# Performance work log

Measured on AMD Instinct MI355X. Metric: run time of the kernel, lower is better.

Reference implementation:

```python
import jax, jax.numpy as jnp
import numpy as np

N_QUBITS = 4
N_LAYERS = 3
DIM = 2 ** N_QUBITS  # 16 amplitudes; qubit 0 is the most-significant bit
BATCH = 262144

# bit of qubit q in basis index: (idx >> (N_QUBITS-1-q)) & 1
_bits = (np.arange(DIM)[:, None] >> np.arange(N_QUBITS - 1, -1, -1)[None, :]) & 1  # [16,4]

# circular CZ entangler diagonal: CZ(0,1),CZ(1,2),CZ(2,3),CZ(0,3)
_sign = np.ones(DIM)
for p, q in [(0, 1), (1, 2), (2, 3), (0, 3)]:
    _sign *= 1.0 - 2.0 * (_bits[:, p] * _bits[:, q])
CZ_DIAG = jnp.asarray(_sign, jnp.complex64)           # [16]
ZMAT = jnp.asarray(1 - 2 * _bits, jnp.float32)        # [16,4], <Z_q> signs


def _rx(t):
    c = jnp.cos(t / 2).astype(jnp.complex64)
    js = (-1j) * jnp.sin(t / 2).astype(jnp.complex64)
    return jnp.stack([jnp.stack([c, js], -1), jnp.stack([js, c], -1)], -2)


def _ry(t):
    c = jnp.cos(t / 2).astype(jnp.complex64)
    s = jnp.sin(t / 2).astype(jnp.complex64)
    return jnp.stack([jnp.stack([c, -s], -1), jnp.stack([s, c], -1)], -2)


def _rz(t):
    ph = jnp.exp(-0.5j * t.astype(jnp.complex64))
    z = jnp.zeros_like(ph)
    return jnp.stack([jnp.stack([ph, z], -1), jnp.stack([z, jnp.conj(ph)], -1)], -2)


def _apply(psi, M, q):
    # psi: [B, 16] complex64, M: [2,2] (shared) or [B,2,2] (per-sample)
    L, R = 2 ** q, 2 ** (N_QUBITS - 1 - q)
    B = psi.shape[0]
    psi = psi.reshape(B, L, 2, R)
    eq = 'ij,bljr->blir' if M.ndim == 2 else 'bij,bljr->blir'
    return jnp.einsum(eq, M, psi).reshape(B, DIM)


def setup_inputs() -> dict:
    key = jax.random.key(0)
    k1, k2 = jax.random.split(key)
    x = jax.random.normal(k1, (BATCH, N_QUBITS), dtype=jnp.float32)
    theta = jax.random.uniform(k2, (1, 3 * (N_LAYERS + 1) * N_QUBITS),
                               minval=0.0, maxval=np.pi, dtype=jnp.float32)
    lmbd = jnp.ones((N_QUBITS * N_LAYERS,), dtype=jnp.float32)
    return {"x": x, "theta": theta, "lmbd": lmbd}


def reference(x, theta, lmbd):
    B = x.shape[0]
    params = theta.reshape(N_LAYERS + 1, N_QUBITS, 3)
    # tiled inputs scaled by trainable lambdas: a[b,l,i] = lmbd[l*4+i] * x[b,i]
    a = lmbd.reshape(N_LAYERS, N_QUBITS)[None] * x[:, None, :]  # [B,3,4]
    # activation = 'linear' -> identity
    psi = jnp.zeros((B, DIM), jnp.complex64).at[:, 0].set(1.0)
    for l in range(N_LAYERS):
        # variational single-qubit rotations (shared across batch)
        for i in range(N_QUBITS):
            psi = _apply(psi, _rx(params[l, i, 0]), i)
            psi = _apply(psi, _ry(params[l, i, 1]), i)
            psi = _apply(psi, _rz(params[l, i, 2]), i)
        # circular CZ entangler (diagonal)
        psi = psi * CZ_DIAG
        # data re-uploading (per-sample angles)
        for i in range(N_QUBITS):
            psi = _apply(psi, _rx(a[:, l, i]), i)
        for i in range(N_QUBITS):
            psi = _apply(psi, _ry(a[:, l, i]), i)
        zang = (a[:, l, 0], a[:, l, 0], a[:, l, 1], a[:, l, 1])
        for i in range(N_QUBITS):
            psi = _apply(psi, _rz(zang[i]), i)
        # trailing variational rotations with last-layer params (applied every layer)
        for i in range(N_QUBITS):
            psi = _apply(psi, _rx(params[N_LAYERS, i, 0]), i)
            psi = _apply(psi, _ry(params[N_LAYERS, i, 1]), i)
            psi = _apply(psi, _rz(params[N_LAYERS, i, 2]), i)
    probs = psi.real ** 2 + psi.imag ** 2  # [B,16]
    return probs @ ZMAT                    # [B,4] <Z_q> expectations
```

## Files before the change

### kernel.cpp

```cpp
#include <hip/hip_runtime.h>

#define BATCH 262144
#define BLOCK 256

typedef float v2 __attribute__((ext_vector_type(2)));

struct c2f { float re, im; };

__device__ __forceinline__ c2f cmul(c2f a, c2f b){
    return { a.re*b.re - a.im*b.im, a.re*b.im + a.im*b.re };
}
__device__ __forceinline__ c2f cmulc(c2f a, c2f b){
    return { a.re*b.re + a.im*b.im, a.im*b.re - a.re*b.im };
}
__device__ __forceinline__ void su2mul(c2f a1, c2f b1, c2f a2, c2f b2, c2f& ao, c2f& bo){
    c2f t1 = cmul(a1, a2), t2 = cmulc(b1, b2);
    ao = { t1.re - t2.re, t1.im - t2.im };
    c2f t3 = cmul(a1, b2), t4 = cmulc(b1, a2);
    bo = { t3.re + t4.re, t3.im + t4.im };
}
__device__ __forceinline__ int czneg(int s){
    int b0 = (s >> 3) & 1, b1 = (s >> 2) & 1, b2 = (s >> 1) & 1, b3 = s & 1;
    return (b0 & b1) ^ (b1 & b2) ^ (b2 & b3) ^ (b0 & b3);
}

__device__ __forceinline__ v2 pkfma(v2 a, v2 b, v2 c){
    return __builtin_elementwise_fma(a, b, c);
}

__global__ __launch_bounds__(BLOCK) void vqc_kernel(
    const float* __restrict__ x,
    const float* __restrict__ theta,
    const float* __restrict__ lmbd,
    float* __restrict__ out)
{
    const int tid = threadIdx.x;
    const int b = blockIdx.x * BLOCK + tid;
    const float4 xr = ((const float4*)x)[b];

    __shared__ float2 sU[4][4][2];
    __shared__ float2 sA[3][4][2];
    __shared__ float2 sPsi0[16];
    __shared__ float  sL[12];

    if (tid < 16) {
        int l = tid >> 2, q = tid & 3;
        float t0 = 0.5f * theta[(l * 4 + q) * 3 + 0];
        float t1 = 0.5f * theta[(l * 4 + q) * 3 + 1];
        float t2 = 0.5f * theta[(l * 4 + q) * 3 + 2];
        float c0, s0, c1, s1, c2v, s2v;
        __sincosf(t0, &s0, &c0);
        __sincosf(t1, &s1, &c1);
        __sincosf(t2, &s2v, &c2v);
        c2f aP = { c1 * c0, s1 * s0 };
        c2f bP = { -s1 * c0, -c1 * s0 };
        c2f ph = { c2v, -s2v };
        c2f aU = cmul(ph, aP);
        c2f bU = cmul(ph, bP);
        sU[l][q][0] = make_float2(aU.re, aU.im);
        sU[l][q][1] = make_float2(bU.re, bU.im);
    }
    if (tid < 12) sL[tid] = lmbd[tid];
    __syncthreads();

    if (tid < 12) {
        int k = tid >> 2, q = tid & 3;
        c2f aW = { sU[3][q][0].x, sU[3][q][0].y };
        c2f bW = { sU[3][q][1].x, sU[3][q][1].y };
        c2f aA = aW, bA = bW;
        if (k < 2) {
            c2f aN = { sU[k + 1][q][0].x, sU[k + 1][q][0].y };
            c2f bN = { sU[k + 1][q][1].x, sU[k + 1][q][1].y };
            su2mul(aN, bN, aW, bW, aA, bA);
        }
        sA[k][q][0] = make_float2(aA.re, aA.im);
        sA[k][q][1] = make_float2(bA.re, bA.im);
    }
    if (tid >= 16 && tid < 32) {
        int s = tid - 16;
        c2f v = { 1.f, 0.f };
        #pragma unroll
        for (int q = 0; q < 4; ++q) {
            int bit = (s >> (3 - q)) & 1;
            c2f a = { sU[0][q][0].x, sU[0][q][0].y };
            c2f b2 = { sU[0][q][1].x, sU[0][q][1].y };
            c2f e = bit ? c2f{ -b2.re, b2.im } : a;
            v = cmul(v, e);
        }
        if (czneg(s)) { v.re = -v.re; v.im = -v.im; }
        sPsi0[s] = make_float2(v.re, v.im);
    }
    __syncthreads();


#define DECLP(n) v2 p##n = { sPsi0[n].x, sPsi0[n].y };
    DECLP(0)  DECLP(1)  DECLP(2)  DECLP(3)
    DECLP(4)  DECLP(5)  DECLP(6)  DECLP(7)
    DECLP(8)  DECLP(9)  DECLP(10) DECLP(11)
    DECLP(12) DECLP(13) DECLP(14) DECLP(15)
#undef DECLP

#define BF(n0,n1) { \
    const v2 q0 = p##n0, q1 = p##n1; \
    const v2 r0 = { -q0.y, q0.x }; \
    const v2 r1 = { -q1.y, q1.x }; \
    v2 t0 = bMi2 * r1; \
    t0 = pkfma(bMr2, q1, t0); \
    t0 = pkfma(aMi2, r0, t0); \
    t0 = pkfma(aMr2, q0, t0); \
    v2 t1 = bMi2 * r0; \
    t1 = pkfma(bMr2, -q0, t1); \
    t1 = pkfma(aMi2, -r1, t1); \
    t1 = pkfma(aMr2, q1, t1); \
    p##n0 = t0; p##n1 = t1; \
}

#define GATE(kk,qq,zq,...) { \
    const float c_ = ch##qq, s_ = sh##qq; \
    const float cz_ = ch##zq, sz_ = sh##zq; \
    const float cc_ = c_*c_, ss_ = s_*s_, cs_ = c_*s_; \
    const float aVr = cc_*cz_ + ss_*sz_, aVi = ss_*cz_ - cc_*sz_; \
    const float bVr = -cs_*(cz_+sz_),  bVi = -cs_*(cz_-sz_); \
    const float2 fa = sA[kk][qq][0], fb = sA[kk][qq][1]; \
    const float aMr = fa.x*aVr - fa.y*aVi - (fb.x*bVr + fb.y*bVi); \
    const float aMi = fa.x*aVi + fa.y*aVr - (fb.y*bVr - fb.x*bVi); \
    const float bMr = fa.x*bVr - fa.y*bVi + (fb.x*aVr + fb.y*aVi); \
    const float bMi = fa.x*bVi + fa.y*bVr + (fb.y*aVr - fb.x*aVi); \
    const v2 aMr2 = { aMr, aMr }, aMi2 = { aMi, aMi }; \
    const v2 bMr2 = { bMr, bMr }, bMi2 = { bMi, bMi }; \
    __VA_ARGS__ \
}

#define CZFLIP \
    p3 = -p3;  p6 = -p6;  p9 = -p9;  p12 = -p12;

#define LAYER(kk, DO_CZ) { \
    const float h0 = 0.5f * sL[kk*4+0] * xr.x; \
    const float h1 = 0.5f * sL[kk*4+1] * xr.y; \
    const float h2 = 0.5f * sL[kk*4+2] * xr.z; \
    const float h3 = 0.5f * sL[kk*4+3] * xr.w; \
    float ch0, sh0, ch1, sh1, ch2, sh2, ch3, sh3; \
    __sincosf(h0, &sh0, &ch0); \
    __sincosf(h1, &sh1, &ch1); \
    __sincosf(h2, &sh2, &ch2); \
    __sincosf(h3, &sh3, &ch3); \
    GATE(kk,0,0, BF(0,8)  BF(1,9)  BF(2,10) BF(3,11) BF(4,12) BF(5,13) BF(6,14)  BF(7,15))  \
    GATE(kk,1,0, BF(0,4)  BF(1,5)  BF(2,6)  BF(3,7)  BF(8,12) BF(9,13) BF(10,14) BF(11,15)) \
    GATE(kk,2,1, BF(0,2)  BF(1,3)  BF(4,6)  BF(5,7)  BF(8,10) BF(9,11) BF(12,14) BF(13,15)) \
    GATE(kk,3,1, BF(0,1)  BF(2,3)  BF(4,5)  BF(6,7)  BF(8,9)  BF(10,11) BF(12,13) BF(14,15))\
    if (DO_CZ) { CZFLIP } \
}

    LAYER(0, 1)
    LAYER(1, 1)
    LAYER(2, 0)

#undef LAYER
#undef GATE
#undef BF
#undef CZFLIP

#define PROB(n) const float m##n = p##n.x*p##n.x + p##n.y*p##n.y;
    PROB(0)  PROB(1)  PROB(2)  PROB(3)
    PROB(4)  PROB(5)  PROB(6)  PROB(7)
    PROB(8)  PROB(9)  PROB(10) PROB(11)
    PROB(12) PROB(13) PROB(14) PROB(15)
#undef PROB

    const float o0 = ((m0+m1)+(m2+m3)+(m4+m5)+(m6+m7))
                   - ((m8+m9)+(m10+m11)+(m12+m13)+(m14+m15));
    const float o1 = ((m0+m1)+(m2+m3)+(m8+m9)+(m10+m11))
                   - ((m4+m5)+(m6+m7)+(m12+m13)+(m14+m15));
    const float o2 = ((m0+m1)+(m4+m5)+(m8+m9)+(m12+m13))
                   - ((m2+m3)+(m6+m7)+(m10+m11)+(m14+m15));
    const float o3 = ((m0+m2)+(m4+m6)+(m8+m10)+(m12+m14))
                   - ((m1+m3)+(m5+m7)+(m9+m11)+(m13+m15));

    ((float4*)out)[b] = make_float4(o0, o1, o2, o3);
}

extern "C" void kernel_launch(void* const* d_in, const int* in_sizes, int n_in,
                              void* d_out, int out_size, void* d_ws, size_t ws_size,
                              hipStream_t stream) {
    const float* x     = (const float*)d_in[0];
    const float* theta = (const float*)d_in[1];
    const float* lmbd  = (const float*)d_in[2];
    float* out = (float*)d_out;
    vqc_kernel<<<dim3(BATCH / BLOCK), dim3(BLOCK), 0, stream>>>(x, theta, lmbd, out);
}
```

Baseline: 71.90 us.

## Process two batch samples per thread and cache gate constants in registers

```diff
diff --git a/kernel.cpp b/kernel.cpp
--- a/kernel.cpp
+++ b/kernel.cpp
@@ -2,6 +2,7 @@
 
 #define BATCH 262144
 #define BLOCK 256
+#define GRID  (BATCH / (BLOCK * 2))
 
 typedef float v2 __attribute__((ext_vector_type(2)));
 
@@ -35,13 +36,15 @@
     float* __restrict__ out)
 {
     const int tid = threadIdx.x;
-    const int b = blockIdx.x * BLOCK + tid;
-    const float4 xr = ((const float4*)x)[b];
+    const int i0 = blockIdx.x * (BLOCK * 2) + tid;
+    const int i1 = i0 + BLOCK;
+    const float4 xrA = ((const float4*)x)[i0];
+    const float4 xrB = ((const float4*)x)[i1];
 
     __shared__ float2 sU[4][4][2];
     __shared__ float2 sA[3][4][2];
     __shared__ float2 sPsi0[16];
-    __shared__ float  sL[12];
+    __shared__ float  sLs[12];
 
     if (tid < 16) {
         int l = tid >> 2, q = tid & 3;
@@ -60,7 +63,7 @@
         sU[l][q][0] = make_float2(aU.re, aU.im);
         sU[l][q][1] = make_float2(bU.re, bU.im);
     }
-    if (tid < 12) sL[tid] = lmbd[tid];
+    if (tid < 12) sLs[tid] = lmbd[tid];
     __syncthreads();
 
     if (tid < 12) {
@@ -92,16 +95,27 @@
     }
     __syncthreads();
 
-
-#define DECLP(n) v2 p##n = { sPsi0[n].x, sPsi0[n].y };
+    float2 rA[3][4][2];
+    #pragma unroll
+    for (int k = 0; k < 3; ++k)
+        #pragma unroll
+        for (int q = 0; q < 4; ++q) {
+            rA[k][q][0] = sA[k][q][0];
+            rA[k][q][1] = sA[k][q][1];
+        }
+    float rL[12];
+    #pragma unroll
+    for (int j = 0; j < 12; ++j) rL[j] = sLs[j];
+
+#define DECLP(n) v2 pA##n = { sPsi0[n].x, sPsi0[n].y }; v2 pB##n = pA##n;
     DECLP(0)  DECLP(1)  DECLP(2)  DECLP(3)
     DECLP(4)  DECLP(5)  DECLP(6)  DECLP(7)
     DECLP(8)  DECLP(9)  DECLP(10) DECLP(11)
     DECLP(12) DECLP(13) DECLP(14) DECLP(15)
 #undef DECLP
 
-#define BF(n0,n1) { \
-    const v2 q0 = p##n0, q1 = p##n1; \
+#define BF(E,n0,n1) { \
+    const v2 q0 = p##E##n0, q1 = p##E##n1; \
     const v2 r0 = { -q0.y, q0.x }; \
     const v2 r1 = { -q1.y, q1.x }; \
     v2 t0 = bMi2 * r1; \
@@ -112,16 +126,16 @@
     t1 = pkfma(bMr2, -q0, t1); \
     t1 = pkfma(aMi2, -r1, t1); \
     t1 = pkfma(aMr2, q1, t1); \
-    p##n0 = t0; p##n1 = t1; \
-}
-
-#define GATE(kk,qq,zq,...) { \
-    const float c_ = ch##qq, s_ = sh##qq; \
-    const float cz_ = ch##zq, sz_ = sh##zq; \
+    p##E##n0 = t0; p##E##n1 = t1; \
+}
+
+#define GATE(E,kk,qq,zq,...) { \
+    const float c_ = ch##E##qq, s_ = sh##E##qq; \
+    const float cz_ = ch##E##zq, sz_ = sh##E##zq; \
     const float cc_ = c_*c_, ss_ = s_*s_, cs_ = c_*s_; \
     const float aVr = cc_*cz_ + ss_*sz_, aVi = ss_*cz_ - cc_*sz_; \
     const float bVr = -cs_*(cz_+sz_),  bVi = -cs_*(cz_-sz_); \
-    const float2 fa = sA[kk][qq][0], fb = sA[kk][qq][1]; \
+    const float2 fa = rA[kk][qq][0], fb = rA[kk][qq][1]; \
     const float aMr = fa.x*aVr - fa.y*aVi - (fb.x*bVr + fb.y*bVi); \
     const float aMi = fa.x*aVi + fa.y*aVr - (fb.y*bVr - fb.x*bVi); \
     const float bMr = fa.x*bVr - fa.y*bVi + (fb.x*aVr + fb.y*aVi); \
@@ -131,24 +145,30 @@
     __VA_ARGS__ \
 }
 
-#define CZFLIP \
-    p3 = -p3;  p6 = -p6;  p9 = -p9;  p12 = -p12;
+#define CZFLIP(E) \
+    p##E##3 = -p##E##3;  p##E##6 = -p##E##6; \
+    p##E##9 = -p##E##9;  p##E##12 = -p##E##12;
 
 #define LAYER(kk, DO_CZ) { \
-    const float h0 = 0.5f * sL[kk*4+0] * xr.x; \
-    const float h1 = 0.5f * sL[kk*4+1] * xr.y; \
-    const float h2 = 0.5f * sL[kk*4+2] * xr.z; \
-    const float h3 = 0.5f * sL[kk*4+3] * xr.w; \
-    float ch0, sh0, ch1, sh1, ch2, sh2, ch3, sh3; \
-    __sincosf(h0, &sh0, &ch0); \
-    __sincosf(h1, &sh1, &ch1); \
-    __sincosf(h2, &sh2, &ch2); \
-    __sincosf(h3, &sh3, &ch3); \
-    GATE(kk,0,0, BF(0,8)  BF(1,9)  BF(2,10) BF(3,11) BF(4,12) BF(5,13) BF(6,14)  BF(7,15))  \
-    GATE(kk,1,0, BF(0,4)  BF(1,5)  BF(2,6)  BF(3,7)  BF(8,12) BF(9,13) BF(10,14) BF(11,15)) \
-    GATE(kk,2,1, BF(0,2)  BF(1,3)  BF(4,6)  BF(5,7)  BF(8,10) BF(9,11) BF(12,14) BF(13,15)) \
-    GATE(kk,3,1, BF(0,1)  BF(2,3)  BF(4,5)  BF(6,7)  BF(8,9)  BF(10,11) BF(12,13) BF(14,15))\
-    if (DO_CZ) { CZFLIP } \
+    float chA0, shA0, chA1, shA1, chA2, shA2, chA3, shA3; \
+    float chB0, shB0, chB1, shB1, chB2, shB2, chB3, shB3; \
+    __sincosf(0.5f * rL[kk*4+0] * xrA.x, &shA0, &chA0); \
+    __sincosf(0.5f * rL[kk*4+1] * xrA.y, &shA1, &chA1); \
+    __sincosf(0.5f * rL[kk*4+2] * xrA.z, &shA2, &chA2); \
+    __sincosf(0.5f * rL[kk*4+3] * xrA.w, &shA3, &chA3); \
+    __sincosf(0.5f * rL[kk*4+0] * xrB.x, &shB0, &chB0); \
+    __sincosf(0.5f * rL[kk*4+1] * xrB.y, &shB1, &chB1); \
+    __sincosf(0.5f * rL[kk*4+2] * xrB.z, &shB2, &chB2); \
+    __sincosf(0.5f * rL[kk*4+3] * xrB.w, &shB3, &chB3); \
+    GATE(A,kk,0,0, BF(A,0,8)  BF(A,1,9)  BF(A,2,10) BF(A,3,11) BF(A,4,12) BF(A,5,13) BF(A,6,14)  BF(A,7,15))  \
+    GATE(B,kk,0,0, BF(B,0,8)  BF(B,1,9)  BF(B,2,10) BF(B,3,11) BF(B,4,12) BF(B,5,13) BF(B,6,14)  BF(B,7,15))  \
+    GATE(A,kk,1,0, BF(A,0,4)  BF(A,1,5)  BF(A,2,6)  BF(A,3,7)  BF(A,8,12) BF(A,9,13) BF(A,10,14) BF(A,11,15)) \
+    GATE(B,kk,1,0, BF(B,0,4)  BF(B,1,5)  BF(B,2,6)  BF(B,3,7)  BF(B,8,12) BF(B,9,13) BF(B,10,14) BF(B,11,15)) \
+    GATE(A,kk,2,1, BF(A,0,2)  BF(A,1,3)  BF(A,4,6)  BF(A,5,7)  BF(A,8,10) BF(A,9,11) BF(A,12,14) BF(A,13,15)) \
+    GATE(B,kk,2,1, BF(B,0,2)  BF(B,1,3)  BF(B,4,6)  BF(B,5,7)  BF(B,8,10) BF(B,9,11) BF(B,12,14) BF(B,13,15)) \
+    GATE(A,kk,3,1, BF(A,0,1)  BF(A,2,3)  BF(A,4,5)  BF(A,6,7)  BF(A,8,9)  BF(A,10,11) BF(A,12,13) BF(A,14,15))\
+    GATE(B,kk,3,1, BF(B,0,1)  BF(B,2,3)  BF(B,4,5)  BF(B,6,7)  BF(B,8,9)  BF(B,10,11) BF(B,12,13) BF(B,14,15))\
+    if (DO_CZ) { CZFLIP(A) CZFLIP(B) } \
 }
 
     LAYER(0, 1)
@@ -160,23 +180,27 @@
 #undef BF
 #undef CZFLIP
 
-#define PROB(n) const float m##n = p##n.x*p##n.x + p##n.y*p##n.y;
-    PROB(0)  PROB(1)  PROB(2)  PROB(3)
-    PROB(4)  PROB(5)  PROB(6)  PROB(7)
-    PROB(8)  PROB(9)  PROB(10) PROB(11)
-    PROB(12) PROB(13) PROB(14) PROB(15)
-#undef PROB
-
-    const float o0 = ((m0+m1)+(m2+m3)+(m4+m5)+(m6+m7))
-                   - ((m8+m9)+(m10+m11)+(m12+m13)+(m14+m15));
-    const float o1 = ((m0+m1)+(m2+m3)+(m8+m9)+(m10+m11))
-                   - ((m4+m5)+(m6+m7)+(m12+m13)+(m14+m15));
-    const float o2 = ((m0+m1)+(m4+m5)+(m8+m9)+(m12+m13))
-                   - ((m2+m3)+(m6+m7)+(m10+m11)+(m14+m15));
-    const float o3 = ((m0+m2)+(m4+m6)+(m8+m10)+(m12+m14))
-                   - ((m1+m3)+(m5+m7)+(m9+m11)+(m13+m15));
-
-    ((float4*)out)[b] = make_float4(o0, o1, o2, o3);
+#define PRB(E,n) const float m##n = p##E##n.x*p##E##n.x + p##E##n.y*p##E##n.y;
+#define EPILOGUE(E, idx) { \
+    PRB(E,0)  PRB(E,1)  PRB(E,2)  PRB(E,3)  \
+    PRB(E,4)  PRB(E,5)  PRB(E,6)  PRB(E,7)  \
+    PRB(E,8)  PRB(E,9)  PRB(E,10) PRB(E,11) \
+    PRB(E,12) PRB(E,13) PRB(E,14) PRB(E,15) \
+    const float o0 = ((m0+m1)+(m2+m3)+(m4+m5)+(m6+m7)) \
+                   - ((m8+m9)+(m10+m11)+(m12+m13)+(m14+m15)); \
+    const float o1 = ((m0+m1)+(m2+m3)+(m8+m9)+(m10+m11)) \
+                   - ((m4+m5)+(m6+m7)+(m12+m13)+(m14+m15)); \
+    const float o2 = ((m0+m1)+(m4+m5)+(m8+m9)+(m12+m13)) \
+                   - ((m2+m3)+(m6+m7)+(m10+m11)+(m14+m15)); \
+    const float o3 = ((m0+m2)+(m4+m6)+(m8+m10)+(m12+m14)) \
+                   - ((m1+m3)+(m5+m7)+(m9+m11)+(m13+m15)); \
+    ((float4*)out)[idx] = make_float4(o0, o1, o2, o3); \
+}
+
+    EPILOGUE(A, i0)
+    EPILOGUE(B, i1)
+#undef EPILOGUE
+#undef PRB
 }
 
 extern "C" void kernel_launch(void* const* d_in, const int* in_sizes, int n_in,
@@ -186,5 +210,5 @@
     const float* theta = (const float*)d_in[1];
     const float* lmbd  = (const float*)d_in[2];
     float* out = (float*)d_out;
-    vqc_kernel<<<dim3(BATCH / BLOCK), dim3(BLOCK), 0, stream>>>(x, theta, lmbd, out);
-}
+    vqc_kernel<<<dim3(GRID), dim3(BLOCK), 0, stream>>>(x, theta, lmbd, out);
+}
```

New measurement: 72.55 us. About the same (+0.9%).
